# Kernel optimization log

Measured on AMD Instinct MI355X. Metric: run time of the kernel, lower is better.

## Reference

```python
import jax, jax.numpy as jnp
import numpy as np
import math

D_MODEL = 1024
N_HEADS = 16
D_K = D_MODEL // N_HEADS
B, S = 2, 2048


def setup_inputs() -> dict:
    key = jax.random.key(0)
    ks = jax.random.split(key, 11)
    sc = 1.0 / math.sqrt(D_MODEL)
    inp = {
        'q': jax.random.normal(ks[0], (B, S, D_MODEL), jnp.float32),
        'k': jax.random.normal(ks[1], (B, S, D_MODEL), jnp.float32),
        'v': jax.random.normal(ks[2], (B, S, D_MODEL), jnp.float32),
        'mask': jnp.tril(jnp.ones((S, S), jnp.int32))[None, None],  # [1,1,S,S] causal
        'W_q': jax.random.normal(ks[3], (D_MODEL, D_MODEL), jnp.float32) * sc,
        'b_q': jnp.zeros((D_MODEL,), jnp.float32),
        'W_k': jax.random.normal(ks[4], (D_MODEL, D_MODEL), jnp.float32) * sc,
        'b_k': jnp.zeros((D_MODEL,), jnp.float32),
        'W_v': jax.random.normal(ks[5], (D_MODEL, D_MODEL), jnp.float32) * sc,
        'b_v': jnp.zeros((D_MODEL,), jnp.float32),
        'W_o': jax.random.normal(ks[6], (D_MODEL, D_MODEL), jnp.float32) * sc,
        'b_o': jnp.zeros((D_MODEL,), jnp.float32),
    }
    return inp


def reference(q, k, v, mask, W_q, b_q, W_k, b_k, W_v, b_v, W_o, b_o):
    # Linear projections then split heads: [B,S,D] -> [B,H,S,d_k]
    def split_heads(x):
        b, s, _ = x.shape
        return x.reshape(b, s, N_HEADS, D_K).transpose(0, 2, 1, 3)

    Q = split_heads(q @ W_q + b_q)
    K = split_heads(k @ W_k + b_k)
    V = split_heads(v @ W_v + b_v)

    scores = jnp.einsum('bhqd,bhkd->bhqk', Q, K) / math.sqrt(D_K)
    scores = jnp.where(mask == 0, jnp.float32(-1e9), scores)
    attn = jax.nn.softmax(scores, axis=-1)  # dropout is identity in eval mode
    out = jnp.einsum('bhqk,bhkd->bhqd', attn, V)
    out = out.transpose(0, 2, 1, 3).reshape(q.shape[0], -1, D_MODEL)
    return out @ W_o + b_o
```

## Files before the change

kernel.cpp:

```cpp
#include <hip/hip_runtime.h>
#include <hip/hip_bf16.h>

#define D_MODEL 1024
#define S_LEN   2048
#define BATCH   2
#define NH      16
#define DK      64

typedef __bf16 bf16_t;
typedef __attribute__((ext_vector_type(8))) __bf16 bf16x8;
typedef __attribute__((ext_vector_type(4))) float f32x4;

#if __has_builtin(__builtin_amdgcn_exp2f)
#define EXP2F(x) __builtin_amdgcn_exp2f(x)
#else
#define EXP2F(x) exp2f(x)
#endif

#define Q_SCALE 0.1803368801111204f

#define GLDS16(gp, lp) __builtin_amdgcn_global_load_lds( \
    (const __attribute__((address_space(1))) void*)(gp), \
    (__attribute__((address_space(3))) void*)(lp), 16, 0, 0)

__global__ void prep_w(const float* __restrict__ Wq, const float* __restrict__ Wk,
                       const float* __restrict__ Wv, const float* __restrict__ Wo,
                       bf16_t* __restrict__ WqkvT, bf16_t* __restrict__ WoT)
{
    __shared__ float t[32][33];
    const int mat = blockIdx.z;
    const int tile = blockIdx.x;
    const int bx = tile & 31, by = tile >> 5;
    const float* in = (mat == 0) ? Wq : (mat == 1) ? Wk : (mat == 2) ? Wv : Wo;
    bf16_t* out = (mat < 3) ? (WqkvT + (long)mat * D_MODEL * D_MODEL) : WoT;
    int tx = threadIdx.x, ty = threadIdx.y;
    int gx = bx * 32, gy = by * 32;
#pragma unroll
    for (int i = 0; i < 32; i += 8)
        t[ty + i][tx] = in[(gy + ty + i) * D_MODEL + gx + tx];
    __syncthreads();
#pragma unroll
    for (int i = 0; i < 32; i += 8)
        out[(gx + ty + i) * D_MODEL + gy + tx] = (bf16_t)t[tx][ty + i];
}

#define BN 128
#define BKT 64

template <int ROWS>
__device__ __forceinline__ void stage_swz(const bf16_t* __restrict__ G, int row0,
                                          int k0, bf16_t* __restrict__ Ls, int tid) {
#pragma unroll
    for (int it = 0; it < ROWS / 32; ++it) {
        int g = it * 256 + tid;
        int row = g >> 3;
        int c = (g & 7) ^ (row & 7);
        GLDS16(&G[(long)(row0 + row) * D_MODEL + k0 + c * 8],
               &Ls[(it * 256 + (tid & ~63)) * 8]);
    }
}

__device__ __forceinline__ bf16x8 frag_swz(const bf16_t* __restrict__ Ls, int row, int cg) {
    return *(const bf16x8*)(&Ls[(row * 8 + (cg ^ (row & 7))) * 8]);
}

__device__ __forceinline__ bf16x8 cvt8(float4 a, float4 b) {
    bf16x8 o;
    o[0] = (bf16_t)a.x; o[1] = (bf16_t)a.y; o[2] = (bf16_t)a.z; o[3] = (bf16_t)a.w;
    o[4] = (bf16_t)b.x; o[5] = (bf16_t)b.y; o[6] = (bf16_t)b.z; o[7] = (bf16_t)b.w;
    return o;
}

#define QM 64
constexpr int QKV_SMEM = (QM * BKT + BN * BKT);
__global__ __launch_bounds__(256) void gemm_qkv(
    const float* __restrict__ qsrc, const float* __restrict__ ksrc,
    const float* __restrict__ vsrc, const bf16_t* __restrict__ WqkvT,
    const float* __restrict__ bq, const float* __restrict__ bk, const float* __restrict__ bv,
    bf16_t* __restrict__ Qw, bf16_t* __restrict__ Kw, bf16_t* __restrict__ Vt)
{
    __shared__ __align__(16) bf16_t smem[QKV_SMEM];
    bf16_t* As = smem;
    bf16_t* Bs = smem + QM * BKT;
    const int z = blockIdx.z;
    const float* A   = (z == 0) ? qsrc : (z == 1) ? ksrc : vsrc;
    const bf16_t* BT = WqkvT + (long)z * D_MODEL * D_MODEL;
    const float* bias = (z == 0) ? bq : (z == 1) ? bk : bv;
    bf16_t* Cb = (z == 0) ? Qw : (z == 1) ? Kw : Vt;
    const float oscale = (z == 0) ? Q_SCALE : 1.0f;

    const int tid  = threadIdx.x;
    const int wave = tid >> 6, lane = tid & 63;
    const int lrow = lane & 15, kgrp = lane >> 4;
    const int wm = (wave >> 1) * 32, wn = (wave & 1) * 64;
    int lin = blockIdx.y * 8 + blockIdx.x;
    int m0 = (lin & 63) * QM;
    int n0 = (lin >> 6) * BN;

    const int ar0 = tid >> 3,         ac0 = tid & 7;
    const int ar1 = (256 + tid) >> 3, ac1 = tid & 7;
    const int as0 = (ar0 * 8 + (ac0 ^ (ar0 & 7))) * 8;
    const int as1 = (ar1 * 8 + (ac1 ^ (ar1 & 7))) * 8;
    const float* arow0 = &A[(long)(m0 + ar0) * D_MODEL + ac0 * 8];
    const float* arow1 = &A[(long)(m0 + ar1) * D_MODEL + ac1 * 8];

    float4 pa0a = *(const float4*)(arow0);
    float4 pa0b = *(const float4*)(arow0 + 4);
    float4 pa1a = *(const float4*)(arow1);
    float4 pa1b = *(const float4*)(arow1 + 4);

    f32x4 acc[2][4] = {};

    for (int k0 = 0; k0 < D_MODEL; k0 += BKT) {
        __syncthreads();
        stage_swz<BN>(BT, n0, k0, Bs, tid);
        *(bf16x8*)(&As[as0]) = cvt8(pa0a, pa0b);
        *(bf16x8*)(&As[as1]) = cvt8(pa1a, pa1b);
        __syncthreads();
        if (k0 + BKT < D_MODEL) {
            pa0a = *(const float4*)(arow0 + k0 + BKT);
            pa0b = *(const float4*)(arow0 + k0 + BKT + 4);
            pa1a = *(const float4*)(arow1 + k0 + BKT);
            pa1b = *(const float4*)(arow1 + k0 + BKT + 4);
        }
#pragma unroll
        for (int kk = 0; kk < 2; ++kk) {
            bf16x8 af[2], bfr[4];
#pragma unroll
            for (int mi = 0; mi < 2; ++mi)
                af[mi] = frag_swz(As, wm + mi * 16 + lrow, kk * 4 + kgrp);
#pragma unroll
            for (int ni = 0; ni < 4; ++ni)
                bfr[ni] = frag_swz(Bs, wn + ni * 16 + lrow, kk * 4 + kgrp);
#pragma unroll
            for (int mi = 0; mi < 2; ++mi)
#pragma unroll
                for (int ni = 0; ni < 4; ++ni)
                    acc[mi][ni] = __builtin_amdgcn_mfma_f32_16x16x32_bf16(af[mi], bfr[ni], acc[mi][ni], 0, 0, 0);
        }
    }

    if (z != 2) {
#pragma unroll
        for (int mi = 0; mi < 2; ++mi)
#pragma unroll
            for (int ni = 0; ni < 4; ++ni) {
                int col = n0 + wn + ni * 16 + lrow;
                float bvf = bias[col];
#pragma unroll
                for (int r = 0; r < 4; ++r) {
                    int row = m0 + wm + mi * 16 + kgrp * 4 + r;
                    float vv = (acc[mi][ni][r] + bvf) * oscale;
                    int b = row >> 11, s = row & (S_LEN - 1);
                    int h = col >> 6, d = col & (DK - 1);
                    Cb[(((long)(b * NH + h) * S_LEN + s) * DK) + d] = (bf16_t)vv;
                }
            }
    } else {
        bf16_t* Ct = smem;
        __syncthreads();
#pragma unroll
        for (int mi = 0; mi < 2; ++mi)
#pragma unroll
            for (int ni = 0; ni < 4; ++ni) {
                int cl = wn + ni * 16 + lrow;
                float bvf = bias[n0 + cl];
#pragma unroll
                for (int r = 0; r < 4; ++r) {
                    int rl = wm + mi * 16 + kgrp * 4 + r;
                    Ct[cl * 72 + rl] = (bf16_t)(acc[mi][ni][r] + bvf);
                }
            }
        __syncthreads();
        const int b = m0 >> 11, sbase = m0 & (S_LEN - 1);
#pragma unroll
        for (int pass = 0; pass < 4; ++pass) {
            int dl = pass * 32 + (tid >> 3);
            int sc = (tid & 7) * 8;
            int colg = n0 + dl;
            int h = colg >> 6, d = colg & (DK - 1);
            bf16_t* dst = Cb + (((long)(b * NH + h) * DK + d) * S_LEN + sbase + sc);
            *(bf16x8*)(dst) = *(const bf16x8*)&Ct[dl * 72 + sc];
        }
    }
}

#define OM 64
__global__ __launch_bounds__(256) void gemm_out(
    const bf16_t* __restrict__ A, const bf16_t* __restrict__ BT,
    const float* __restrict__ bias, float* __restrict__ Cf)
{
    __shared__ __align__(16) bf16_t As[OM * BKT];
    __shared__ __align__(16) bf16_t Bs[BN * BKT];
    const int tid  = threadIdx.x;
    const int wave = tid >> 6, lane = tid & 63;
    const int lrow = lane & 15, kgrp = lane >> 4;
    const int wm = (wave >> 1) * 32, wn = (wave & 1) * 64;
    int lin = blockIdx.y * 8 + blockIdx.x;
    int m0 = (lin & 63) * OM;
    int n0 = (lin >> 6) * BN;

    f32x4 acc[2][4] = {};

    for (int k0 = 0; k0 < D_MODEL; k0 += BKT) {
        stage_swz<OM>(A, m0, k0, As, tid);
        stage_swz<BN>(BT, n0, k0, Bs, tid);
        __syncthreads();
#pragma unroll
        for (int kk = 0; kk < 2; ++kk) {
            bf16x8 af[2], bfr[4];
#pragma unroll
            for (int mi = 0; mi < 2; ++mi)
                af[mi] = frag_swz(As, wm + mi * 16 + lrow, kk * 4 + kgrp);
#pragma unroll
            for (int ni = 0; ni < 4; ++ni)
                bfr[ni] = frag_swz(Bs, wn + ni * 16 + lrow, kk * 4 + kgrp);
#pragma unroll
            for (int mi = 0; mi < 2; ++mi)
#pragma unroll
                for (int ni = 0; ni < 4; ++ni)
                    acc[mi][ni] = __builtin_amdgcn_mfma_f32_16x16x32_bf16(af[mi], bfr[ni], acc[mi][ni], 0, 0, 0);
        }
        __syncthreads();
    }

#pragma unroll
    for (int mi = 0; mi < 2; ++mi)
#pragma unroll
        for (int ni = 0; ni < 4; ++ni) {
            int col = n0 + wn + ni * 16 + lrow;
            float bvf = bias[col];
#pragma unroll
            for (int r = 0; r < 4; ++r) {
                int row = m0 + wm + mi * 16 + kgrp * 4 + r;
                Cf[(long)row * D_MODEL + col] = acc[mi][ni][r] + bvf;
            }
        }
}

__device__ __forceinline__ void stage_k(const bf16_t* __restrict__ Kt,
                                        bf16_t* __restrict__ Ls, int tid) {
#pragma unroll
    for (int it = 0; it < 2; ++it) {
        int g = it * 256 + tid;
        int row = g >> 3;
        int srow = 32 * ((row >> 4) & 1) + 8 * ((row >> 2) & 3)
                 + 4 * (row >> 5) + (row & 3);
        int c = (g & 7) ^ (row & 7);
        GLDS16(&Kt[(long)srow * DK + c * 8], &Ls[(it * 256 + (tid & ~63)) * 8]);
    }
}

__device__ __forceinline__ void stage_v(const bf16_t* __restrict__ Vth, int j0,
                                        bf16_t* __restrict__ Ls, int tid) {
#pragma unroll
    for (int it = 0; it < 2; ++it) {
        int g = it * 256 + tid;
        int row = g >> 3;
        int c = (g & 7) ^ (row & 7);
        GLDS16(&Vth[(long)row * S_LEN + j0 + c * 8], &Ls[(it * 256 + (tid & ~63)) * 8]);
    }
}

__device__ __forceinline__ void attn_one_qtile(
    int qi, int bh, int wave, int lrow, int kgrp, int tid,
    const bf16_t* __restrict__ Qh, const bf16_t* __restrict__ Kh,
    const bf16_t* __restrict__ Vth, bf16_t* __restrict__ O,
    bf16_t (*Ks)[64 * 64], bf16_t (*Vs)[64 * 64])
{
    const int qrow = qi * 64 + wave * 16;
    const int qg = qrow + lrow;

    bf16x8 qf[2];
#pragma unroll
    for (int kk = 0; kk < 2; ++kk)
        qf[kk] = *(const bf16x8*)(&Qh[(qrow + lrow) * DK + kk * 32 + kgrp * 8]);

    f32x4 acc[4] = {};
    float lsum = 0.f;

    const int nt = qi + 1;

    stage_k(Kh, Ks[0], tid);
    stage_v(Vth, 0, Vs[0], tid);
    __syncthreads();

    for (int t = 0; t < nt; ++t) {
        const int cur = t & 1;
        if (t + 1 < nt) {
            stage_k(Kh + (long)(t + 1) * 64 * DK, Ks[cur ^ 1], tid);
            stage_v(Vth, (t + 1) * 64, Vs[cur ^ 1], tid);
        }
        const bf16_t* Kc = Ks[cur];
        const bf16_t* Vc = Vs[cur];
        const int j0 = t * 64;

        f32x4 sc[4] = {};
#pragma unroll
        for (int kk = 0; kk < 2; ++kk)
#pragma unroll
            for (int ni = 0; ni < 4; ++ni) {
                bf16x8 kf = frag_swz(Kc, ni * 16 + lrow, kk * 4 + kgrp);
                sc[ni] = __builtin_amdgcn_mfma_f32_16x16x32_bf16(kf, qf[kk], sc[ni], 0, 0, 0);
            }

        float pb[4][4];
        const bool needmask = (j0 + 63 > qrow);
        if (needmask) {
#pragma unroll
            for (int ni = 0; ni < 4; ++ni) {
                const int cb = j0 + (ni & 1) * 32 + kgrp * 8 + ((ni >> 1) << 2);
#pragma unroll
                for (int r = 0; r < 4; ++r) {
                    float pv = EXP2F(sc[ni][r]);
                    if (cb + r > qg) pv = 0.f;
                    lsum += pv;
                    pb[ni][r] = pv;
                }
            }
        } else {
#pragma unroll
            for (int ni = 0; ni < 4; ++ni)
#pragma unroll
                for (int r = 0; r < 4; ++r) {
                    float pv = EXP2F(sc[ni][r]);
                    lsum += pv;
                    pb[ni][r] = pv;
                }
        }

        bf16x8 pf0, pf1;
#pragma unroll
        for (int r = 0; r < 4; ++r) {
            pf0[r]     = (bf16_t)pb[0][r];
            pf0[r + 4] = (bf16_t)pb[2][r];
            pf1[r]     = (bf16_t)pb[1][r];
            pf1[r + 4] = (bf16_t)pb[3][r];
        }

#pragma unroll
        for (int di = 0; di < 4; ++di) {
            bf16x8 vf = frag_swz(Vc, di * 16 + lrow, kgrp);
            acc[di] = __builtin_amdgcn_mfma_f32_16x16x32_bf16(pf0, vf, acc[di], 0, 0, 0);
        }
#pragma unroll
        for (int di = 0; di < 4; ++di) {
            bf16x8 vf = frag_swz(Vc, di * 16 + lrow, 4 + kgrp);
            acc[di] = __builtin_amdgcn_mfma_f32_16x16x32_bf16(pf1, vf, acc[di], 0, 0, 0);
        }

        __syncthreads();
    }

    lsum += __shfl_xor(lsum, 16);
    lsum += __shfl_xor(lsum, 32);

    const int b = bh >> 4, h = bh & (NH - 1);
#pragma unroll
    for (int r = 0; r < 4; ++r) {
        float inv = 1.f / __shfl(lsum, kgrp * 4 + r);
        int s = qrow + kgrp * 4 + r;
#pragma unroll
        for (int di = 0; di < 4; ++di) {
            int d = di * 16 + lrow;
            O[((long)(b * S_LEN + s)) * D_MODEL + h * DK + d] = (bf16_t)(acc[di][r] * inv);
        }
    }
}

__global__ __launch_bounds__(256, 2) void attn_kernel(
    const bf16_t* __restrict__ Q, const bf16_t* __restrict__ K,
    const bf16_t* __restrict__ Vt, bf16_t* __restrict__ O)
{
    __shared__ __align__(16) bf16_t Ks[2][64 * 64];
    __shared__ __align__(16) bf16_t Vs[2][64 * 64];

    const int bh = blockIdx.y;
    const int p  = blockIdx.x;
    const int tid = threadIdx.x, wave = tid >> 6, lane = tid & 63;
    const int lrow = lane & 15, kgrp = lane >> 4;

    const bf16_t* Qh  = Q  + (long)bh * S_LEN * DK;
    const bf16_t* Kh  = K  + (long)bh * S_LEN * DK;
    const bf16_t* Vth = Vt + (long)bh * DK * S_LEN;

    attn_one_qtile(31 - p, bh, wave, lrow, kgrp, tid,
                   Qh, Kh, Vth, O, Ks, Vs);
    attn_one_qtile(p, bh, wave, lrow, kgrp, tid,
                   Qh, Kh, Vth, O, Ks, Vs);
}

extern "C" void kernel_launch(void* const* d_in, const int* in_sizes, int n_in,
                              void* d_out, int out_size, void* d_ws, size_t ws_size,
                              hipStream_t stream) {
    const float* q  = (const float*)d_in[0];
    const float* k  = (const float*)d_in[1];
    const float* v  = (const float*)d_in[2];
    const float* Wq = (const float*)d_in[4];
    const float* bq = (const float*)d_in[5];
    const float* Wk = (const float*)d_in[6];
    const float* bk = (const float*)d_in[7];
    const float* Wv = (const float*)d_in[8];
    const float* bv = (const float*)d_in[9];
    const float* Wo = (const float*)d_in[10];
    const float* bo = (const float*)d_in[11];

    char* ws = (char*)d_ws;
    const size_t Mi = 1024 * 1024;
    bf16_t* WqkvT = (bf16_t*)(ws);
    bf16_t* WoT   = (bf16_t*)(ws + 6 * Mi);
    bf16_t* Qw    = (bf16_t*)(ws + 8 * Mi);
    bf16_t* Kw    = (bf16_t*)(ws + 16 * Mi);
    bf16_t* Vtw   = (bf16_t*)(ws + 24 * Mi);
    bf16_t* Aw    = (bf16_t*)(ws + 32 * Mi);

    dim3 tb(32, 8);
    prep_w<<<dim3(1024, 1, 4), tb, 0, stream>>>(Wq, Wk, Wv, Wo, WqkvT, WoT);

    gemm_qkv<<<dim3(8, (BATCH * S_LEN) / QM, 3), 256, 0, stream>>>(
        q, k, v, WqkvT, bq, bk, bv, Qw, Kw, Vtw);

    attn_kernel<<<dim3(16, BATCH * NH), 256, 0, stream>>>(Qw, Kw, Vtw, Aw);

    gemm_out<<<dim3(8, (BATCH * S_LEN) / OM), 256, 0, stream>>>(
        Aw, WoT, bo, (float*)d_out);
}
```

Before: 218.9 us.

## Share K/V tile loads between paired causal query tiles in attention

Instead of processing the two paired query tiles (31-p and p) sequentially, each streaming K/V from scratch, the block now walks K/V tiles once for the longer tile and computes the shorter tile's contribution on the same staged K/V while t < ntB. This removes the redundant global-to-LDS staging and barriers of the second pass. In exchange, two sets of accumulators and Q fragments are live at once, which raises register pressure and may reduce occupancy under launch_bounds(256,2).

```diff
diff --git a/kernel.cpp b/kernel.cpp
--- a/kernel.cpp
+++ b/kernel.cpp
@@ -262,99 +262,72 @@
     }
 }
 
-__device__ __forceinline__ void attn_one_qtile(
-    int qi, int bh, int wave, int lrow, int kgrp, int tid,
-    const bf16_t* __restrict__ Qh, const bf16_t* __restrict__ Kh,
-    const bf16_t* __restrict__ Vth, bf16_t* __restrict__ O,
-    bf16_t (*Ks)[64 * 64], bf16_t (*Vs)[64 * 64])
-{
-    const int qrow = qi * 64 + wave * 16;
-    const int qg = qrow + lrow;
-
-    bf16x8 qf[2];
+__device__ __forceinline__ void attn_tile_compute(
+    int qrow, int qg, int j0, const bf16x8* __restrict__ qf,
+    const bf16_t* __restrict__ Kc, const bf16_t* __restrict__ Vc,
+    int lrow, int kgrp, f32x4 (&acc)[4], float& lsum)
+{
+    f32x4 sc[4] = {};
 #pragma unroll
     for (int kk = 0; kk < 2; ++kk)
-        qf[kk] = *(const bf16x8*)(&Qh[(qrow + lrow) * DK + kk * 32 + kgrp * 8]);
-
-    f32x4 acc[4] = {};
-    float lsum = 0.f;
-
-    const int nt = qi + 1;
-
-    stage_k(Kh, Ks[0], tid);
-    stage_v(Vth, 0, Vs[0], tid);
-    __syncthreads();
-
-    for (int t = 0; t < nt; ++t) {
-        const int cur = t & 1;
-        if (t + 1 < nt) {
-            stage_k(Kh + (long)(t + 1) * 64 * DK, Ks[cur ^ 1], tid);
-            stage_v(Vth, (t + 1) * 64, Vs[cur ^ 1], tid);
-        }
-        const bf16_t* Kc = Ks[cur];
-        const bf16_t* Vc = Vs[cur];
-        const int j0 = t * 64;
-
-        f32x4 sc[4] = {};
-#pragma unroll
-        for (int kk = 0; kk < 2; ++kk)
-#pragma unroll
-            for (int ni = 0; ni < 4; ++ni) {
-                bf16x8 kf = frag_swz(Kc, ni * 16 + lrow, kk * 4 + kgrp);
-                sc[ni] = __builtin_amdgcn_mfma_f32_16x16x32_bf16(kf, qf[kk], sc[ni], 0, 0, 0);
+#pragma unroll
+        for (int ni = 0; ni < 4; ++ni) {
+            bf16x8 kf = frag_swz(Kc, ni * 16 + lrow, kk * 4 + kgrp);
+            sc[ni] = __builtin_amdgcn_mfma_f32_16x16x32_bf16(kf, qf[kk], sc[ni], 0, 0, 0);
+        }
+
+    float pb[4][4];
+    const bool needmask = (j0 + 63 > qrow);
+    if (needmask) {
+#pragma unroll
+        for (int ni = 0; ni < 4; ++ni) {
+            const int cb = j0 + (ni & 1) * 32 + kgrp * 8 + ((ni >> 1) << 2);
+#pragma unroll
+            for (int r = 0; r < 4; ++r) {
+                float pv = EXP2F(sc[ni][r]);
+                if (cb + r > qg) pv = 0.f;
+                lsum += pv;
+                pb[ni][r] = pv;
             }
-
-        float pb[4][4];
-        const bool needmask = (j0 + 63 > qrow);
-        if (needmask) {
-#pragma unroll
-            for (int ni = 0; ni < 4; ++ni) {
-                const int cb = j0 + (ni & 1) * 32 + kgrp * 8 + ((ni >> 1) << 2);
-#pragma unroll
-                for (int r = 0; r < 4; ++r) {
-                    float pv = EXP2F(sc[ni][r]);
-                    if (cb + r > qg) pv = 0.f;
-                    lsum += pv;
-                    pb[ni][r] = pv;
-                }
+        }
+    } else {
+#pragma unroll
+        for (int ni = 0; ni < 4; ++ni)
+#pragma unroll
+            for (int r = 0; r < 4; ++r) {
+                float pv = EXP2F(sc[ni][r]);
+                lsum += pv;
+                pb[ni][r] = pv;
             }
-        } else {
-#pragma unroll
-            for (int ni = 0; ni < 4; ++ni)
-#pragma unroll
-                for (int r = 0; r < 4; ++r) {
-                    float pv = EXP2F(sc[ni][r]);
-                    lsum += pv;
-                    pb[ni][r] = pv;
-                }
-        }
-
-        bf16x8 pf0, pf1;
-#pragma unroll
-        for (int r = 0; r < 4; ++r) {
-            pf0[r]     = (bf16_t)pb[0][r];
-            pf0[r + 4] = (bf16_t)pb[2][r];
-            pf1[r]     = (bf16_t)pb[1][r];
-            pf1[r + 4] = (bf16_t)pb[3][r];
-        }
-
-#pragma unroll
-        for (int di = 0; di < 4; ++di) {
-            bf16x8 vf = frag_swz(Vc, di * 16 + lrow, kgrp);
-            acc[di] = __builtin_amdgcn_mfma_f32_16x16x32_bf16(pf0, vf, acc[di], 0, 0, 0);
-        }
-#pragma unroll
-        for (int di = 0; di < 4; ++di) {
-            bf16x8 vf = frag_swz(Vc, di * 16 + lrow, 4 + kgrp);
-            acc[di] = __builtin_amdgcn_mfma_f32_16x16x32_bf16(pf1, vf, acc[di], 0, 0, 0);
-        }
-
-        __syncthreads();
-    }
-
+    }
+
+    bf16x8 pf0, pf1;
+#pragma unroll
+    for (int r = 0; r < 4; ++r) {
+        pf0[r]     = (bf16_t)pb[0][r];
+        pf0[r + 4] = (bf16_t)pb[2][r];
+        pf1[r]     = (bf16_t)pb[1][r];
+        pf1[r + 4] = (bf16_t)pb[3][r];
+    }
+
+#pragma unroll
+    for (int di = 0; di < 4; ++di) {
+        bf16x8 vf = frag_swz(Vc, di * 16 + lrow, kgrp);
+        acc[di] = __builtin_amdgcn_mfma_f32_16x16x32_bf16(pf0, vf, acc[di], 0, 0, 0);
+    }
+#pragma unroll
+    for (int di = 0; di < 4; ++di) {
+        bf16x8 vf = frag_swz(Vc, di * 16 + lrow, 4 + kgrp);
+        acc[di] = __builtin_amdgcn_mfma_f32_16x16x32_bf16(pf1, vf, acc[di], 0, 0, 0);
+    }
+}
+
+__device__ __forceinline__ void attn_epilogue(
+    int bh, int qrow, int lrow, int kgrp,
+    f32x4 (&acc)[4], float lsum, bf16_t* __restrict__ O)
+{
     lsum += __shfl_xor(lsum, 16);
     lsum += __shfl_xor(lsum, 32);
-
     const int b = bh >> 4, h = bh & (NH - 1);
 #pragma unroll
     for (int r = 0; r < 4; ++r) {
@@ -384,10 +357,45 @@
     const bf16_t* Kh  = K  + (long)bh * S_LEN * DK;
     const bf16_t* Vth = Vt + (long)bh * DK * S_LEN;
 
-    attn_one_qtile(31 - p, bh, wave, lrow, kgrp, tid,
-                   Qh, Kh, Vth, O, Ks, Vs);
-    attn_one_qtile(p, bh, wave, lrow, kgrp, tid,
-                   Qh, Kh, Vth, O, Ks, Vs);
+    const int qiA = 31 - p, qiB = p;
+    const int qrowA = qiA * 64 + wave * 16, qgA = qrowA + lrow;
+    const int qrowB = qiB * 64 + wave * 16, qgB = qrowB + lrow;
+    const int ntA = qiA + 1;
+    const int ntB = qiB + 1;
+
+    bf16x8 qfA[2], qfB[2];
+#pragma unroll
+    for (int kk = 0; kk < 2; ++kk) {
+        qfA[kk] = *(const bf16x8*)(&Qh[(qrowA + lrow) * DK + kk * 32 + kgrp * 8]);
+        qfB[kk] = *(const bf16x8*)(&Qh[(qrowB + lrow) * DK + kk * 32 + kgrp * 8]);
+    }
+
+    f32x4 accA[4] = {}, accB[4] = {};
+    float lsumA = 0.f, lsumB = 0.f;
+
+    stage_k(Kh, Ks[0], tid);
+    stage_v(Vth, 0, Vs[0], tid);
+    __syncthreads();
+
+    for (int t = 0; t < ntA; ++t) {
+        const int cur = t & 1;
+        if (t + 1 < ntA) {
+            stage_k(Kh + (long)(t + 1) * 64 * DK, Ks[cur ^ 1], tid);
+            stage_v(Vth, (t + 1) * 64, Vs[cur ^ 1], tid);
+        }
+        const bf16_t* Kc = Ks[cur];
+        const bf16_t* Vc = Vs[cur];
+        const int j0 = t * 64;
+
+        attn_tile_compute(qrowA, qgA, j0, qfA, Kc, Vc, lrow, kgrp, accA, lsumA);
+        if (t < ntB)
+            attn_tile_compute(qrowB, qgB, j0, qfB, Kc, Vc, lrow, kgrp, accB, lsumB);
+
+        __syncthreads();
+    }
+
+    attn_epilogue(bh, qrowA, lrow, kgrp, accA, lsumA, O);
+    attn_epilogue(bh, qrowB, lrow, kgrp, accB, lsumB, O);
 }
 
 extern "C" void kernel_launch(void* const* d_in, const int* in_sizes, int n_in,
```

After: 216.3 us. Within noise of the previous version (-1.2%).
